# Optimization experiments

Hardware: AMD Instinct MI355X
Metric: run time of the kernel (lower is better)

## Reference

```python
import jax, jax.numpy as jnp
import numpy as np

N = 100000   # nodes
E = 1000000  # edges
D = 64       # in_features
D_OUT = 64   # out_features


def setup_inputs() -> dict:
    key = jax.random.key(0)
    k1, k2, k3, k4, k5, k6 = jax.random.split(key, 6)
    h = jax.random.normal(k1, (N, D), dtype=jnp.float32)          # current node features ndata['h']
    i = jax.random.normal(k2, (N, D), dtype=jnp.float32)          # initial features ndata['i']
    edge_src = jax.random.randint(k3, (E,), 0, N, dtype=jnp.int32)
    edge_dst = jax.random.randint(k4, (E,), 0, N, dtype=jnp.int32)
    edge_w = jax.random.uniform(k5, (E,), dtype=jnp.float32)      # scalar edge weight edata['x']
    stdv = 1.0 / np.sqrt(D_OUT)
    weight = jax.random.uniform(k6, (2 * D, D_OUT), dtype=jnp.float32,
                                minval=-stdv, maxval=stdv)        # variant=True -> in = 2*D
    return {
        "h": h, "i": i, "weight": weight, "edge_w": edge_w,
        "lamda": jnp.float32(0.5), "alpha": jnp.float32(0.1),
        "edge_src": edge_src, "edge_dst": edge_dst, "layer_idx": 4,
    }


def reference(h, i, weight, edge_w, lamda, alpha, edge_src, edge_dst, layer_idx):
    # theta = min(1, log(lamda/layer_idx + 1))
    theta = jnp.minimum(jnp.float32(1.0), jnp.log(lamda / layer_idx + 1.0))
    # update_all(u_mul_e('h','x','m'), sum('m','h')): edge-weighted gather-scatter SpMM
    m = h[edge_src] * edge_w[:, None]                 # [E, D]
    h_agg = jax.ops.segment_sum(m, edge_dst, num_segments=h.shape[0])  # [N, D]
    # variant=True branch
    support = jnp.concatenate([h_agg, i], axis=1)     # [N, 2D]
    r = (1.0 - alpha) * h_agg + alpha * i             # [N, D]
    out = theta * (support @ weight) + (1.0 - theta) * r
    # residual=True
    out = out + i
    return out
```

## Files before the change

### kernel.cpp

```cpp
#include <hip/hip_runtime.h>
#include <math.h>


#define DFEAT 64
#define NBINS 512
#define CAP   4096
#define CHUNK 4096
#define TPB   512

typedef unsigned long long u64;
typedef __attribute__((ext_vector_type(8))) short bf16x8;
typedef __attribute__((ext_vector_type(4))) float f32x4;

__device__ inline unsigned short to_bf16(float f) {
    unsigned u = __float_as_uint(f);
    u += 0x7FFF + ((u >> 16) & 1);
    return (unsigned short)(u >> 16);
}
__device__ inline float bf_up(unsigned short s) {
    return __uint_as_float(((unsigned)s) << 16);
}

__global__ __launch_bounds__(256) void cvt_h_kernel(
    const float* __restrict__ h, ushort* __restrict__ h16, int total4) {
    int i = blockIdx.x * 256 + threadIdx.x;
    if (i < total4) {
        float4 v = ((const float4*)h)[i];
        ushort4 o;
        o.x = to_bf16(v.x); o.y = to_bf16(v.y);
        o.z = to_bf16(v.z); o.w = to_bf16(v.w);
        ((ushort4*)h16)[i] = o;
    }
}

__global__ __launch_bounds__(512) void bin_fill_kernel(
    const int* __restrict__ e_src, const int* __restrict__ e_dst,
    const float* __restrict__ e_w, int* __restrict__ gcur,
    u64* __restrict__ bucket, int E) {
    __shared__ u64 staging[CHUNK];
    __shared__ unsigned short binOf[CHUNK];
    __shared__ int hist[NBINS], offs[NBINS], gbase[NBINS];
    __shared__ int cur[NBINS], part[TPB];

    int tid = threadIdx.x;
    int e0 = blockIdx.x * CHUNK;
    int cc = min(CHUNK, E - e0);

    hist[tid] = 0;
    __syncthreads();

    int d[8], s[8];
    float w[8];
#pragma unroll
    for (int j = 0; j < 8; ++j) {
        int e = e0 + j * TPB + tid;
        if (e < E) { d[j] = e_dst[e]; s[j] = e_src[e]; w[j] = e_w[e]; }
        else d[j] = -1;
    }
#pragma unroll
    for (int j = 0; j < 8; ++j)
        if (d[j] >= 0) atomicAdd(&hist[d[j] >> 8], 1);
    __syncthreads();

    int v = hist[tid];
    part[tid] = v;
    __syncthreads();
    for (int ofs = 1; ofs < TPB; ofs <<= 1) {
        int t = (tid >= ofs) ? part[tid - ofs] : 0;
        __syncthreads();
        part[tid] += t;
        __syncthreads();
    }
    int excl = part[tid] - v;
    offs[tid] = excl; cur[tid] = excl;
    __syncthreads();

#pragma unroll
    for (int j = 0; j < 8; ++j) {
        if (d[j] >= 0) {
            int bb = d[j] >> 8;
            int p = atomicAdd(&cur[bb], 1);
            unsigned lo = (unsigned)s[j] | ((unsigned)(d[j] & 255) << 24);
            staging[p] = ((u64)(unsigned)__float_as_int(w[j]) << 32) | lo;
            binOf[p] = (unsigned short)bb;
        }
    }
    __syncthreads();

    {
        int c = hist[tid];
        gbase[tid] = (c > 0) ? atomicAdd(&gcur[tid], c) : 0;
    }
    __syncthreads();

#pragma unroll
    for (int j = 0; j < 8; ++j) {
        int p = j * TPB + tid;
        if (p < cc) {
            int bb = binOf[p];
            bucket[(size_t)bb * CAP + gbase[bb] + (p - offs[bb])] = staging[p];
        }
    }
}

__global__ __launch_bounds__(512) void sort_gather_kernel(
    const ushort* __restrict__ h16, const u64* __restrict__ bucket,
    const int* __restrict__ gcur, float* __restrict__ agg, int N) {
    __shared__ u64 sorted[CAP];
    __shared__ int hist[256], start[256], cur[256], part[256];

    int tid = threadIdx.x;
    int bin = blockIdx.x >> 1;
    int half = blockIdx.x & 1;
    int cnt = gcur[bin];
    const u64* bk = bucket + (size_t)bin * CAP;

    if (tid < 256) hist[tid] = 0;
    __syncthreads();

    for (int p = tid; p < cnt; p += 512)
        atomicAdd(&hist[((unsigned)bk[p]) >> 24], 1);
    __syncthreads();

    int v = 0;
    if (tid < 256) { v = hist[tid]; part[tid] = v; }
    __syncthreads();
    for (int ofs = 1; ofs < 256; ofs <<= 1) {
        int t = 0;
        if (tid < 256 && tid >= ofs) t = part[tid - ofs];
        __syncthreads();
        if (tid < 256) part[tid] += t;
        __syncthreads();
    }
    if (tid < 256) { start[tid] = part[tid] - v; cur[tid] = part[tid] - v; }
    __syncthreads();

    for (int p = tid; p < cnt; p += 512) {
        u64 e = bk[p];
        int pos = atomicAdd(&cur[((unsigned)e) >> 24], 1);
        sorted[pos] = e;
    }
    __syncthreads();

    int lane = tid & 63, wv = tid >> 6;
    int g = lane >> 4, m = lane & 15;
    int base = bin << 8;
    int nn = min(256, N - base);

    for (int nl = half + 2 * wv; nl < nn; nl += 16) {
        int d = hist[nl];
        int b0 = start[nl];
        float a0 = 0.f, a1 = 0.f, a2 = 0.f, a3 = 0.f;
        for (int t0 = 0; t0 < d; t0 += 16) {
#pragma unroll
            for (int s = 0; s < 4; ++s) {
                int idx = t0 + s * 4 + g;
                u64 e = sorted[b0 + min(idx, d - 1)];
                float wt = (idx < d) ? __int_as_float((int)(e >> 32)) : 0.f;
                int src = ((unsigned)e) & 0xFFFFFF;
                ushort4 hv = *(const ushort4*)(h16 + (size_t)src * DFEAT + m * 4);
                a0 += wt * bf_up(hv.x);
                a1 += wt * bf_up(hv.y);
                a2 += wt * bf_up(hv.z);
                a3 += wt * bf_up(hv.w);
            }
        }
        a0 += __shfl_xor(a0, 16); a1 += __shfl_xor(a1, 16);
        a2 += __shfl_xor(a2, 16); a3 += __shfl_xor(a3, 16);
        a0 += __shfl_xor(a0, 32); a1 += __shfl_xor(a1, 32);
        a2 += __shfl_xor(a2, 32); a3 += __shfl_xor(a3, 32);
        if (g == 0) {
            float4 o; o.x = a0; o.y = a1; o.z = a2; o.w = a3;
            *(float4*)(agg + (size_t)(base + nl) * DFEAT + m * 4) = o;
        }
    }
}

__global__ __launch_bounds__(256) void epilogue_mfma_kernel(
    const float* agg, const float* __restrict__ ifeat,
    const float* __restrict__ weight,
    const float* __restrict__ lamda_p, const float* __restrict__ alpha_p,
    const int* __restrict__ layer_p,
    float* out, int N, int total_waves) {
    int lane = threadIdx.x & 63;
    int wave = (blockIdx.x * 256 + threadIdx.x) >> 6;
    int q = lane >> 4;
    int m = lane & 15;

    bf16x8 bW[4][4];
#pragma unroll
    for (int c = 0; c < 4; ++c)
#pragma unroll
        for (int s = 0; s < 4; ++s)
#pragma unroll
            for (int j = 0; j < 8; ++j)
                bW[c][s][j] = (short)to_bf16(weight[(s * 32 + q * 8 + j) * DFEAT + c * 16 + m]);

    float alf = alpha_p[0];
    float theta = fminf(1.0f, logf(lamda_p[0] / (float)layer_p[0] + 1.0f));

    int ntiles = (N + 15) >> 4;
    for (int t = wave; t < ntiles; t += total_waves) {
        int rbase = t << 4;
        int arow = min(rbase + m, N - 1);
        const float* ap = agg + (size_t)arow * DFEAT;
        const float* ip = ifeat + (size_t)arow * DFEAT;

        f32x4 acc[4] = {{0.f, 0.f, 0.f, 0.f}, {0.f, 0.f, 0.f, 0.f},
                        {0.f, 0.f, 0.f, 0.f}, {0.f, 0.f, 0.f, 0.f}};
#pragma unroll
        for (int s = 0; s < 4; ++s) {
            const float* p = ((s < 2) ? ap : ip) + ((s & 1) ? 32 : 0) + q * 8;
            float4 v0 = *(const float4*)p;
            float4 v1 = *(const float4*)(p + 4);
            bf16x8 fa;
            fa[0] = (short)to_bf16(v0.x); fa[1] = (short)to_bf16(v0.y);
            fa[2] = (short)to_bf16(v0.z); fa[3] = (short)to_bf16(v0.w);
            fa[4] = (short)to_bf16(v1.x); fa[5] = (short)to_bf16(v1.y);
            fa[6] = (short)to_bf16(v1.z); fa[7] = (short)to_bf16(v1.w);
#pragma unroll
            for (int c = 0; c < 4; ++c)
                acc[c] = __builtin_amdgcn_mfma_f32_16x16x32_bf16(fa, bW[c][s], acc[c], 0, 0, 0);
        }

#pragma unroll
        for (int c = 0; c < 4; ++c) {
            int col = c * 16 + m;
#pragma unroll
            for (int r = 0; r < 4; ++r) {
                int row = rbase + q * 4 + r;
                if (row < N) {
                    size_t o = (size_t)row * DFEAT + col;
                    float av = agg[o], iv = ifeat[o];
                    out[o] = theta * acc[c][r] +
                             (1.f - theta) * ((1.f - alf) * av + alf * iv) + iv;
                }
            }
        }
    }
}

extern "C" void kernel_launch(void* const* d_in, const int* in_sizes, int n_in,
                              void* d_out, int out_size, void* d_ws, size_t ws_size,
                              hipStream_t stream) {
    const float* h       = (const float*)d_in[0];
    const float* ifeat   = (const float*)d_in[1];
    const float* weight  = (const float*)d_in[2];
    const float* edge_w  = (const float*)d_in[3];
    const float* lamda_p = (const float*)d_in[4];
    const float* alpha_p = (const float*)d_in[5];
    const int*   e_src   = (const int*)d_in[6];
    const int*   e_dst   = (const int*)d_in[7];
    const int*   layer_p = (const int*)d_in[8];
    float* out = (float*)d_out;

    int N = in_sizes[0] / DFEAT;
    int E = in_sizes[3];
    int nbins = (N + 255) >> 8;

    int* gcur = (int*)d_ws;
    u64* bucket = (u64*)((char*)d_ws + 4096);
    ushort* h16 = (ushort*)((char*)bucket + (size_t)nbins * CAP * sizeof(u64));

    float* agg = out;

    hipMemsetAsync(gcur, 0, NBINS * sizeof(int), stream);

    int total4 = N * DFEAT / 4;
    cvt_h_kernel<<<(total4 + 255) / 256, 256, 0, stream>>>(h, h16, total4);

    bin_fill_kernel<<<(E + CHUNK - 1) / CHUNK, TPB, 0, stream>>>(
        e_src, e_dst, edge_w, gcur, bucket, E);

    sort_gather_kernel<<<nbins * 2, 512, 0, stream>>>(h16, bucket, gcur, agg, N);

    int epi_blocks = 512;
    epilogue_mfma_kernel<<<epi_blocks, 256, 0, stream>>>(
        agg, ifeat, weight, lamda_p, alpha_p, layer_p, out, N, epi_blocks * 4);
}
```

Baseline: 179.1 us.

## Fuse SpMM aggregation with MFMA epilogue via shared-memory atomics per 128-node bin

Shrinks bins to 128 destination nodes and merges the bf16 conversion of h and weight into the binning kernel. The per-bin sort and per-node gather reduction are replaced by LDS float atomics into a padded shared aggregate tile, which the same block then feeds directly into the MFMA epilogue. This removes two kernel launches, the global round trip of the aggregate, and the in-block counting sort. In exchange it relies on LDS atomic throughput and contention, and bins with more edges than the 2048 capacity would overflow.

```diff
diff --git a/kernel.cpp b/kernel.cpp
--- a/kernel.cpp
+++ b/kernel.cpp
@@ -3,10 +3,12 @@
 
 
 #define DFEAT 64
-#define NBINS 512
-#define CAP   4096
+#define BINSZ 128
+#define NBINS 1024
+#define CAP   2048
 #define CHUNK 4096
 #define TPB   512
+#define APAD  68
 
 typedef unsigned long long u64;
 typedef __attribute__((ext_vector_type(8))) short bf16x8;
@@ -21,32 +23,38 @@
     return __uint_as_float(((unsigned)s) << 16);
 }
 
-__global__ __launch_bounds__(256) void cvt_h_kernel(
-    const float* __restrict__ h, ushort* __restrict__ h16, int total4) {
-    int i = blockIdx.x * 256 + threadIdx.x;
-    if (i < total4) {
+__global__ __launch_bounds__(512) void bin_fill_kernel(
+    const float* __restrict__ h, const float* __restrict__ weight,
+    const int* __restrict__ e_src, const int* __restrict__ e_dst,
+    const float* __restrict__ e_w, int* __restrict__ gcur,
+    u64* __restrict__ bucket, ushort* __restrict__ h16,
+    ushort* __restrict__ w16, int E, int total4) {
+    __shared__ u64 staging[CHUNK];
+    __shared__ unsigned short binOf[CHUNK];
+    __shared__ int hist[NBINS], offs[NBINS], gbase[NBINS], cur[NBINS];
+    __shared__ int part[TPB];
+
+    int tid = threadIdx.x;
+    int gid = blockIdx.x * TPB + tid;
+    int nthreads = gridDim.x * TPB;
+
+    for (int i = gid; i < total4; i += nthreads) {
         float4 v = ((const float4*)h)[i];
         ushort4 o;
         o.x = to_bf16(v.x); o.y = to_bf16(v.y);
         o.z = to_bf16(v.z); o.w = to_bf16(v.w);
         ((ushort4*)h16)[i] = o;
     }
-}
-
-__global__ __launch_bounds__(512) void bin_fill_kernel(
-    const int* __restrict__ e_src, const int* __restrict__ e_dst,
-    const float* __restrict__ e_w, int* __restrict__ gcur,
-    u64* __restrict__ bucket, int E) {
-    __shared__ u64 staging[CHUNK];
-    __shared__ unsigned short binOf[CHUNK];
-    __shared__ int hist[NBINS], offs[NBINS], gbase[NBINS];
-    __shared__ int cur[NBINS], part[TPB];
-
-    int tid = threadIdx.x;
+    if (gid < 8192) {
+        int j = gid & 7, l = (gid >> 3) & 63, cs = gid >> 9;
+        int c = cs >> 2, s = cs & 3, q = l >> 4, m = l & 15;
+        w16[gid] = to_bf16(weight[(s * 32 + q * 8 + j) * DFEAT + c * 16 + m]);
+    }
+
     int e0 = blockIdx.x * CHUNK;
     int cc = min(CHUNK, E - e0);
 
-    hist[tid] = 0;
+    hist[tid] = 0; hist[tid + 512] = 0;
     __syncthreads();
 
     int d[8], s[8];
@@ -59,11 +67,11 @@
     }
 #pragma unroll
     for (int j = 0; j < 8; ++j)
-        if (d[j] >= 0) atomicAdd(&hist[d[j] >> 8], 1);
-    __syncthreads();
-
-    int v = hist[tid];
-    part[tid] = v;
+        if (d[j] >= 0) atomicAdd(&hist[d[j] >> 7], 1);
+    __syncthreads();
+
+    int a = hist[2 * tid], b = hist[2 * tid + 1];
+    part[tid] = a + b;
     __syncthreads();
     for (int ofs = 1; ofs < TPB; ofs <<= 1) {
         int t = (tid >= ofs) ? part[tid - ofs] : 0;
@@ -71,25 +79,26 @@
         part[tid] += t;
         __syncthreads();
     }
-    int excl = part[tid] - v;
-    offs[tid] = excl; cur[tid] = excl;
+    int excl = part[tid] - (a + b);
+    offs[2 * tid] = excl;         cur[2 * tid] = excl;
+    offs[2 * tid + 1] = excl + a; cur[2 * tid + 1] = excl + a;
     __syncthreads();
 
 #pragma unroll
     for (int j = 0; j < 8; ++j) {
         if (d[j] >= 0) {
-            int bb = d[j] >> 8;
+            int bb = d[j] >> 7;
             int p = atomicAdd(&cur[bb], 1);
-            unsigned lo = (unsigned)s[j] | ((unsigned)(d[j] & 255) << 24);
+            unsigned lo = (unsigned)s[j] | ((unsigned)(d[j] & 127) << 24);
             staging[p] = ((u64)(unsigned)__float_as_int(w[j]) << 32) | lo;
             binOf[p] = (unsigned short)bb;
         }
     }
     __syncthreads();
 
-    {
-        int c = hist[tid];
-        gbase[tid] = (c > 0) ? atomicAdd(&gcur[tid], c) : 0;
+    for (int t = tid; t < NBINS; t += TPB) {
+        int c = hist[t];
+        gbase[t] = (c > 0) ? atomicAdd(&gcur[t], c) : 0;
     }
     __syncthreads();
 
@@ -103,138 +112,104 @@
     }
 }
 
-__global__ __launch_bounds__(512) void sort_gather_kernel(
+__global__ __launch_bounds__(512, 6) void spmm_epi_kernel(
     const ushort* __restrict__ h16, const u64* __restrict__ bucket,
-    const int* __restrict__ gcur, float* __restrict__ agg, int N) {
-    __shared__ u64 sorted[CAP];
-    __shared__ int hist[256], start[256], cur[256], part[256];
-
-    int tid = threadIdx.x;
-    int bin = blockIdx.x >> 1;
-    int half = blockIdx.x & 1;
-    int cnt = gcur[bin];
-    const u64* bk = bucket + (size_t)bin * CAP;
-
-    if (tid < 256) hist[tid] = 0;
-    __syncthreads();
-
-    for (int p = tid; p < cnt; p += 512)
-        atomicAdd(&hist[((unsigned)bk[p]) >> 24], 1);
-    __syncthreads();
-
-    int v = 0;
-    if (tid < 256) { v = hist[tid]; part[tid] = v; }
-    __syncthreads();
-    for (int ofs = 1; ofs < 256; ofs <<= 1) {
-        int t = 0;
-        if (tid < 256 && tid >= ofs) t = part[tid - ofs];
-        __syncthreads();
-        if (tid < 256) part[tid] += t;
-        __syncthreads();
-    }
-    if (tid < 256) { start[tid] = part[tid] - v; cur[tid] = part[tid] - v; }
-    __syncthreads();
-
-    for (int p = tid; p < cnt; p += 512) {
-        u64 e = bk[p];
-        int pos = atomicAdd(&cur[((unsigned)e) >> 24], 1);
-        sorted[pos] = e;
-    }
-    __syncthreads();
-
-    int lane = tid & 63, wv = tid >> 6;
-    int g = lane >> 4, m = lane & 15;
-    int base = bin << 8;
-    int nn = min(256, N - base);
-
-    for (int nl = half + 2 * wv; nl < nn; nl += 16) {
-        int d = hist[nl];
-        int b0 = start[nl];
-        float a0 = 0.f, a1 = 0.f, a2 = 0.f, a3 = 0.f;
-        for (int t0 = 0; t0 < d; t0 += 16) {
-#pragma unroll
-            for (int s = 0; s < 4; ++s) {
-                int idx = t0 + s * 4 + g;
-                u64 e = sorted[b0 + min(idx, d - 1)];
-                float wt = (idx < d) ? __int_as_float((int)(e >> 32)) : 0.f;
-                int src = ((unsigned)e) & 0xFFFFFF;
-                ushort4 hv = *(const ushort4*)(h16 + (size_t)src * DFEAT + m * 4);
-                a0 += wt * bf_up(hv.x);
-                a1 += wt * bf_up(hv.y);
-                a2 += wt * bf_up(hv.z);
-                a3 += wt * bf_up(hv.w);
-            }
-        }
-        a0 += __shfl_xor(a0, 16); a1 += __shfl_xor(a1, 16);
-        a2 += __shfl_xor(a2, 16); a3 += __shfl_xor(a3, 16);
-        a0 += __shfl_xor(a0, 32); a1 += __shfl_xor(a1, 32);
-        a2 += __shfl_xor(a2, 32); a3 += __shfl_xor(a3, 32);
-        if (g == 0) {
-            float4 o; o.x = a0; o.y = a1; o.z = a2; o.w = a3;
-            *(float4*)(agg + (size_t)(base + nl) * DFEAT + m * 4) = o;
-        }
-    }
-}
-
-__global__ __launch_bounds__(256) void epilogue_mfma_kernel(
-    const float* agg, const float* __restrict__ ifeat,
-    const float* __restrict__ weight,
+    const int* __restrict__ gcur, const ushort* __restrict__ w16,
+    const float* __restrict__ ifeat,
     const float* __restrict__ lamda_p, const float* __restrict__ alpha_p,
     const int* __restrict__ layer_p,
-    float* out, int N, int total_waves) {
-    int lane = threadIdx.x & 63;
-    int wave = (blockIdx.x * 256 + threadIdx.x) >> 6;
-    int q = lane >> 4;
-    int m = lane & 15;
-
-    bf16x8 bW[4][4];
-#pragma unroll
-    for (int c = 0; c < 4; ++c)
-#pragma unroll
-        for (int s = 0; s < 4; ++s)
-#pragma unroll
-            for (int j = 0; j < 8; ++j)
-                bW[c][s][j] = (short)to_bf16(weight[(s * 32 + q * 8 + j) * DFEAT + c * 16 + m]);
+    float* __restrict__ out, int N) {
+    __shared__ float agg[BINSZ * APAD];
+    __shared__ ushort sW[8192];
+
+    int tid = threadIdx.x;
+    int lane = tid & 63, wv = tid >> 6;
+    int bin = blockIdx.x;
+    int base = bin << 7;
+
+    for (int i = tid; i < BINSZ * APAD; i += TPB) agg[i] = 0.f;
+    for (int i = tid; i < 4096; i += TPB)
+        ((unsigned*)sW)[i] = ((const unsigned*)w16)[i];
+    int cnt = gcur[bin];
+    __syncthreads();
+
+    {
+        int half = lane >> 5;
+        int k = lane & 31;
+        const u64* bk = bucket + (size_t)bin * CAP;
+        for (int e0 = wv * 8; e0 < cnt; e0 += 64) {
+#pragma unroll
+            for (int j = 0; j < 4; ++j) {
+                int idx = e0 + 2 * j + half;
+                u64 e = bk[min(idx, cnt - 1)];
+                float wt = (idx < cnt) ? __int_as_float((int)(e >> 32)) : 0.f;
+                int src = ((unsigned)e) & 0xFFFFFF;
+                int dl = (((unsigned)e) >> 24) & 127;
+                ushort2 hv = *(const ushort2*)(h16 + (size_t)src * DFEAT + 2 * k);
+                atomicAdd(&agg[dl * APAD + 2 * k], wt * bf_up(hv.x));
+                atomicAdd(&agg[dl * APAD + 2 * k + 1], wt * bf_up(hv.y));
+            }
+        }
+    }
+    __syncthreads();
 
     float alf = alpha_p[0];
     float theta = fminf(1.0f, logf(lamda_p[0] / (float)layer_p[0] + 1.0f));
-
-    int ntiles = (N + 15) >> 4;
-    for (int t = wave; t < ntiles; t += total_waves) {
-        int rbase = t << 4;
-        int arow = min(rbase + m, N - 1);
-        const float* ap = agg + (size_t)arow * DFEAT;
-        const float* ip = ifeat + (size_t)arow * DFEAT;
-
-        f32x4 acc[4] = {{0.f, 0.f, 0.f, 0.f}, {0.f, 0.f, 0.f, 0.f},
-                        {0.f, 0.f, 0.f, 0.f}, {0.f, 0.f, 0.f, 0.f}};
-#pragma unroll
-        for (int s = 0; s < 4; ++s) {
-            const float* p = ((s < 2) ? ap : ip) + ((s & 1) ? 32 : 0) + q * 8;
-            float4 v0 = *(const float4*)p;
-            float4 v1 = *(const float4*)(p + 4);
+    int q = lane >> 4, m = lane & 15;
+    int rL = wv * 16 + m;
+    int rG = base + rL;
+
+    f32x4 acc[4] = {{0.f, 0.f, 0.f, 0.f}, {0.f, 0.f, 0.f, 0.f},
+                    {0.f, 0.f, 0.f, 0.f}, {0.f, 0.f, 0.f, 0.f}};
+
+#pragma unroll
+    for (int s = 0; s < 2; ++s) {
+        const float* p = &agg[rL * APAD + s * 32 + q * 8];
+        f32x4 v0 = *(const f32x4*)p;
+        f32x4 v1 = *(const f32x4*)(p + 4);
+        bf16x8 fa;
+        fa[0] = (short)to_bf16(v0[0]); fa[1] = (short)to_bf16(v0[1]);
+        fa[2] = (short)to_bf16(v0[2]); fa[3] = (short)to_bf16(v0[3]);
+        fa[4] = (short)to_bf16(v1[0]); fa[5] = (short)to_bf16(v1[1]);
+        fa[6] = (short)to_bf16(v1[2]); fa[7] = (short)to_bf16(v1[3]);
+#pragma unroll
+        for (int c = 0; c < 4; ++c) {
+            bf16x8 bB = *(const bf16x8*)(sW + ((c * 4 + s) * 64 + lane) * 8);
+            acc[c] = __builtin_amdgcn_mfma_f32_16x16x32_bf16(fa, bB, acc[c], 0, 0, 0);
+        }
+    }
+    {
+        const float* ip = ifeat + (size_t)min(rG, N - 1) * DFEAT;
+#pragma unroll
+        for (int s = 0; s < 2; ++s) {
+            float4 v0 = *(const float4*)(ip + s * 32 + q * 8);
+            float4 v1 = *(const float4*)(ip + s * 32 + q * 8 + 4);
             bf16x8 fa;
             fa[0] = (short)to_bf16(v0.x); fa[1] = (short)to_bf16(v0.y);
             fa[2] = (short)to_bf16(v0.z); fa[3] = (short)to_bf16(v0.w);
             fa[4] = (short)to_bf16(v1.x); fa[5] = (short)to_bf16(v1.y);
             fa[6] = (short)to_bf16(v1.z); fa[7] = (short)to_bf16(v1.w);
 #pragma unroll
-            for (int c = 0; c < 4; ++c)
-                acc[c] = __builtin_amdgcn_mfma_f32_16x16x32_bf16(fa, bW[c][s], acc[c], 0, 0, 0);
-        }
-
-#pragma unroll
-        for (int c = 0; c < 4; ++c) {
-            int col = c * 16 + m;
-#pragma unroll
-            for (int r = 0; r < 4; ++r) {
-                int row = rbase + q * 4 + r;
-                if (row < N) {
-                    size_t o = (size_t)row * DFEAT + col;
-                    float av = agg[o], iv = ifeat[o];
-                    out[o] = theta * acc[c][r] +
-                             (1.f - theta) * ((1.f - alf) * av + alf * iv) + iv;
-                }
+            for (int c = 0; c < 4; ++c) {
+                bf16x8 bB = *(const bf16x8*)(sW + ((c * 4 + s + 2) * 64 + lane) * 8);
+                acc[c] = __builtin_amdgcn_mfma_f32_16x16x32_bf16(fa, bB, acc[c], 0, 0, 0);
+            }
+        }
+    }
+
+#pragma unroll
+    for (int c = 0; c < 4; ++c) {
+        int col = c * 16 + m;
+#pragma unroll
+        for (int r = 0; r < 4; ++r) {
+            int rowL = wv * 16 + q * 4 + r;
+            int row = base + rowL;
+            if (row < N) {
+                float av = agg[rowL * APAD + col];
+                float iv = ifeat[(size_t)row * DFEAT + col];
+                out[(size_t)row * DFEAT + col] =
+                    theta * acc[c][r] +
+                    (1.f - theta) * ((1.f - alf) * av + alf * iv) + iv;
             }
         }
     }
@@ -256,25 +231,19 @@
 
     int N = in_sizes[0] / DFEAT;
     int E = in_sizes[3];
-    int nbins = (N + 255) >> 8;
+    int nbins = (N + BINSZ - 1) >> 7;
 
     int* gcur = (int*)d_ws;
     u64* bucket = (u64*)((char*)d_ws + 4096);
-    ushort* h16 = (ushort*)((char*)bucket + (size_t)nbins * CAP * sizeof(u64));
-
-    float* agg = out;
+    ushort* h16 = (ushort*)((char*)bucket + (size_t)NBINS * CAP * sizeof(u64));
+    ushort* w16 = h16 + (size_t)N * DFEAT;
 
     hipMemsetAsync(gcur, 0, NBINS * sizeof(int), stream);
 
     int total4 = N * DFEAT / 4;
-    cvt_h_kernel<<<(total4 + 255) / 256, 256, 0, stream>>>(h, h16, total4);
-
     bin_fill_kernel<<<(E + CHUNK - 1) / CHUNK, TPB, 0, stream>>>(
-        e_src, e_dst, edge_w, gcur, bucket, E);
-
-    sort_gather_kernel<<<nbins * 2, 512, 0, stream>>>(h16, bucket, gcur, agg, N);
-
-    int epi_blocks = 512;
-    epilogue_mfma_kernel<<<epi_blocks, 256, 0, stream>>>(
-        agg, ifeat, weight, lamda_p, alpha_p, layer_p, out, N, epi_blocks * 4);
-}
+        h, weight, e_src, e_dst, edge_w, gcur, bucket, h16, w16, E, total4);
+
+    spmm_epi_kernel<<<nbins, TPB, 0, stream>>>(
+        h16, bucket, gcur, w16, ifeat, lamda_p, alpha_p, layer_p, out, N);
+}
```

After: 543.2 us. 3.03x slower.
